# Performance work log

Hardware: AMD Instinct MI355X
Metric: run time of the kernel (lower is better)

The kernel has to match this reference:

```python
import jax, jax.numpy as jnp
import numpy as np

WS = 15
PAD = WS // 2
BN_EPS = 1e-5


def _unfold2d(a, ws):
    # a: (b, t, c, H, W) already padded -> (b, t, c, h, w, ws, ws), stride-1 windows
    h = a.shape[3] - ws + 1
    w = a.shape[4] - ws + 1
    ih = (jnp.arange(h)[:, None] + jnp.arange(ws)[None, :])  # (h, ws)
    iw = (jnp.arange(w)[:, None] + jnp.arange(ws)[None, :])  # (w, ws)
    return a[:, :, :, ih[:, None, :, None], iw[None, :, None, :]]


def setup_inputs() -> dict:
    key = jax.random.key(0)
    ks = jax.random.split(key, 11)
    b, t_mem, c, h, w = 2, 2, 256, 32, 32
    s = 0.05
    return {
        "x": jax.random.normal(ks[0], (b, c, h, w), jnp.float32),
        "mem": jax.random.normal(ks[1], (b, t_mem, c, h, w), jnp.float32),
        "w_qk": jax.random.normal(ks[2], (c // 8, c), jnp.float32) * s,
        "w_qv": jax.random.normal(ks[3], (c // 2, c), jnp.float32) * s,
        "w_mk": jax.random.normal(ks[4], (c // 8, c), jnp.float32) * s,
        "w_mv": jax.random.normal(ks[5], (c // 2, c), jnp.float32) * s,
        "w_smooth": jax.random.normal(ks[6], (c, c), jnp.float32) * s,
        "bn_gamma": jax.random.uniform(ks[7], (c,), jnp.float32, 0.5, 1.5),
        "bn_beta": jax.random.normal(ks[8], (c,), jnp.float32) * 0.1,
        "bn_mean": jnp.zeros((c,), jnp.float32),
        "bn_var": jnp.ones((c,), jnp.float32),
    }


def reference(x, mem, w_qk, w_qv, w_mk, w_mv, w_smooth, bn_gamma, bn_beta, bn_mean, bn_var):
    # mem <- cat([x, mem]) along time: (b, t, c, h, w)
    mem = jnp.concatenate([x[:, None], mem], axis=1)
    b, t, c, h, w = mem.shape

    # 1x1 convs == per-pixel matmuls
    query_k = jnp.einsum('bchw,oc->bohw', x, w_qk)          # (b, c/8, h, w)
    query_v = jnp.einsum('bchw,oc->bohw', x, w_qv)          # (b, c/2, h, w); Dropout2d(p=0) is identity
    mem_k = jnp.einsum('btchw,oc->btohw', mem, w_mk)        # (b, t, c/8, h, w)
    mem_v = jnp.einsum('btchw,oc->btohw', mem, w_mv)        # (b, t, c/2, h, w)

    pad = [(0, 0), (0, 0), (0, 0), (PAD, PAD), (PAD, PAD)]
    unf_k = _unfold2d(jnp.pad(mem_k, pad), WS)              # (b, t, c/8, h, w, ws, ws)
    unf_v = _unfold2d(jnp.pad(mem_v, pad), WS)              # (b, t, c/2, h, w, ws, ws)

    attn = jnp.einsum('bchw,btchwxy->bhwtxy', query_k, unf_k)
    attn = attn.reshape(b, h, w, t * WS * WS)
    # NOTE: faithful to original: softmax over dim=2 (the spatial w axis), not over keys
    attn = jax.nn.softmax(attn, axis=2)

    unf_v = jnp.transpose(unf_v, (0, 2, 3, 4, 1, 5, 6)).reshape(b, c // 2, h, w, t * WS * WS)
    mem_out = jnp.einsum('bhwk,bchwk->bchw', attn, unf_v)   # (b, c/2, h, w)

    feat = jnp.concatenate([query_v, mem_out], axis=1)      # (b, c, h, w)
    y = jnp.einsum('bchw,oc->bohw', feat, w_smooth)
    # BatchNorm2d in eval mode (running stats) + ReLU
    inv = bn_gamma / jnp.sqrt(bn_var + BN_EPS)
    y = y * inv[None, :, None, None] + (bn_beta - bn_mean * inv)[None, :, None, None]
    return jax.nn.relu(y)
```

## Files before the change

kernel.cpp:

```cpp
#include <hip/hip_runtime.h>
#include <math.h>

#define HWSZ 1024
#define HH 32
#define WW 32
#define C 256
#define CK 32
#define CV 128
#define T 3
#define WSZ 15
#define PADSZ 7
#define PADDED 46
#define PP (PADDED*PADDED)
#define KK (T*WSZ*WSZ)
#define B 2
#define NOUT 160
#define KC 32
#define PIXT 32
#define NPART 15

static const size_t OFF_QK   = 0;
static const size_t OFF_QV   = 65536;
static const size_t OFF_MK   = 327680;
static const size_t OFF_MV   = 733952;
static const size_t OFF_PART = 2359040;

__global__ __launch_bounds__(256) void k_proj(
    const float* __restrict__ x, const float* __restrict__ mem,
    const float* __restrict__ w_qk, const float* __restrict__ w_qv,
    const float* __restrict__ w_mk, const float* __restrict__ w_mv,
    float* __restrict__ ws)
{
    __shared__ float inT[KC][PIXT];
    __shared__ float wT[NOUT][KC + 1];

    int jb   = blockIdx.x >> 5;
    int rowt = blockIdx.x & 31;
    int tid  = threadIdx.x;
    int tx   = tid & 7;
    int ty   = tid >> 3;

    int b, t;
    const float *wk, *wv;
    bool isq;
    if (jb < 6) { b = jb / 3; t = jb % 3; wk = w_mk; wv = w_mv; isq = false; }
    else        { b = jb - 6; t = 0;      wk = w_qk; wv = w_qv; isq = true;  }

    const float* src = (t == 0)
        ? (x + ((size_t)b * C) * HWSZ)
        : (mem + ((size_t)(b * (T - 1) + (t - 1)) * C) * HWSZ);
    int hw0 = rowt * WW;

    float* mk = ws + OFF_MK;
    float* mv = ws + OFF_MV;
    size_t bt = (size_t)(b * T + t);

    if (!isq) {
        int yp = rowt + PADSZ;
        for (int f = tid; f < 448 + 1792; f += 256) {
            if (f < 448) {
                int c = f >> 4, sc = f & 15;
                if (sc < 14) {
                    int col = (sc < 7) ? sc : sc + 25;
                    mk[(bt * PP + yp * PADDED + col) * CK + c] = 0.f;
                }
            } else {
                int g = f - 448;
                int sc = g >> 7, c = g & 127;
                int col = (sc < 7) ? sc : sc + 25;
                mv[(bt * PP + yp * PADDED + col) * CV + c] = 0.f;
            }
        }
        if (rowt < 14) {
            int pr = (rowt < 7) ? rowt : rowt + 32;
            for (int f = tid; f < 1472 + 5888; f += 256) {
                if (f < 1472) {
                    int col = f >> 5, c = f & 31;
                    mk[(bt * PP + pr * PADDED + col) * CK + c] = 0.f;
                } else {
                    int g = f - 1472;
                    int col = g >> 7, c = g & 127;
                    mv[(bt * PP + pr * PADDED + col) * CV + c] = 0.f;
                }
            }
        }
    }

    float acc[5][4];
    #pragma unroll
    for (int j = 0; j < 5; j++)
        #pragma unroll
        for (int i = 0; i < 4; i++) acc[j][i] = 0.f;

    for (int c0 = 0; c0 < C; c0 += KC) {
        {
            int cc = tid >> 3;
            int p4 = (tid & 7) * 4;
            float4 v = *(const float4*)&src[(size_t)(c0 + cc) * HWSZ + hw0 + p4];
            inT[cc][p4 + 0] = v.x; inT[cc][p4 + 1] = v.y;
            inT[cc][p4 + 2] = v.z; inT[cc][p4 + 3] = v.w;
        }
        #pragma unroll
        for (int j = 0; j < 5; j++) {
            int f  = tid + j * 256;
            int o  = f >> 3;
            int c4 = (f & 7) * 4;
            const float* wr = (o < CK) ? (wk + (size_t)o * C) : (wv + (size_t)(o - CK) * C);
            float4 v = *(const float4*)&wr[c0 + c4];
            wT[o][c4 + 0] = v.x; wT[o][c4 + 1] = v.y;
            wT[o][c4 + 2] = v.z; wT[o][c4 + 3] = v.w;
        }
        __syncthreads();

        #pragma unroll 8
        for (int k = 0; k < KC; k++) {
            float4 iv = *(const float4*)&inT[k][tx * 4];
            #pragma unroll
            for (int j = 0; j < 5; j++) {
                float wv_ = wT[ty * 5 + j][k];
                acc[j][0] += wv_ * iv.x; acc[j][1] += wv_ * iv.y;
                acc[j][2] += wv_ * iv.z; acc[j][3] += wv_ * iv.w;
            }
        }
        __syncthreads();
    }

    int hq = rowt, yp = hq + PADSZ;
    #pragma unroll
    for (int j = 0; j < 5; j++) {
        int o = ty * 5 + j;
        #pragma unroll
        for (int i = 0; i < 4; i++) {
            int wq = tx * 4 + i;
            float v = acc[j][i];
            if (!isq) {
                int xp = wq + PADSZ;
                if (o < CK)
                    mk[(bt * PP + yp * PADDED + xp) * CK + o] = v;
                else
                    mv[(bt * PP + yp * PADDED + xp) * CV + (o - CK)] = v;
            } else {
                int hw = hq * WW + wq;
                if (o < CK) ws[OFF_QK + ((size_t)b * HWSZ + hw) * CK + o] = v;
                else        ws[OFF_QV + ((size_t)(b * CV + (o - CK))) * HWSZ + hw] = v;
            }
        }
    }
}

__global__ __launch_bounds__(256, 4) void k_attn_av(
    const float* __restrict__ qk, const float* __restrict__ mk,
    const float* __restrict__ mv, float* __restrict__ part)
{
    __shared__ float al[2][WSZ][WW];

    int blk = blockIdx.x;
    int xcd = blk & 7;
    int loc = blk >> 3;
    int xg  = loc % 5;
    int t   = (loc % 15) / 5;
    int bh  = xcd * 8 + loc / 15;
    int b   = bh >> 5, hq = bh & 31;
    int tid = threadIdx.x;

    const float* mkb = mk + (size_t)(b * T + t) * PP * CK;
    const float* mvb = mv + (size_t)(b * T + t) * PP * CV;

    int w  = tid & 31;
    int ty = tid >> 5;

    float4 q[8];
    {
        const float* qrow = qk + ((size_t)(b * HWSZ + hq * WW + w)) * CK;
        #pragma unroll
        for (int i = 0; i < 8; i++) q[i] = *(const float4*)&qrow[i * 4];
    }

    int cq = tid & 31;
    int wg = tid >> 5;
    int c0 = cq * 4;
    int w0 = wg * 4;

    float acc[4][4];
    #pragma unroll
    for (int ci = 0; ci < 4; ci++)
        #pragma unroll
        for (int wi = 0; wi < 4; wi++) acc[ci][wi] = 0.f;

    int yy0 = ty, yy1r = (ty + 8 < WSZ) ? ty + 8 : WSZ - 1;
    bool has1 = (ty + 8 < WSZ);

    #pragma unroll 1
    for (int xi = 0; xi < 3; xi++) {
        int xx = xg * 3 + xi;
        int buf = xi & 1;
        const float* mkrow = mkb + (size_t)(hq + xx) * PADDED * CK;
        const float* vrow  = mvb + (size_t)(hq + xx) * PADDED * CV + c0;

        float s0 = 0.f, s1 = 0.f;
        {
            const float* k0 = mkrow + (size_t)(w + yy0) * CK;
            const float* k1 = mkrow + (size_t)(w + yy1r) * CK;
            #pragma unroll
            for (int cc = 0; cc < 8; cc++) {
                float4 m0 = *(const float4*)&k0[cc * 4];
                float4 m1 = *(const float4*)&k1[cc * 4];
                s0 += q[cc].x * m0.x + q[cc].y * m0.y + q[cc].z * m0.z + q[cc].w * m0.w;
                s1 += q[cc].x * m1.x + q[cc].y * m1.y + q[cc].z * m1.z + q[cc].w * m1.w;
            }
        }

        float4 vw[18];
        #pragma unroll
        for (int i = 0; i < 18; i++)
            vw[i] = *(const float4*)&vrow[(size_t)(w0 + i) * CV];

        {
            float m0 = s0, m1 = s1;
            #pragma unroll
            for (int d = 1; d < 32; d <<= 1) {
                m0 = fmaxf(m0, __shfl_xor(m0, d, 32));
                m1 = fmaxf(m1, __shfl_xor(m1, d, 32));
            }
            float e0 = __expf(s0 - m0), e1 = __expf(s1 - m1);
            float t0 = e0, t1 = e1;
            #pragma unroll
            for (int d = 1; d < 32; d <<= 1) {
                t0 += __shfl_xor(t0, d, 32);
                t1 += __shfl_xor(t1, d, 32);
            }
            al[buf][yy0][w] = e0 / t0;
            if (has1) al[buf][yy1r][w] = e1 / t1;
        }
        __syncthreads();

        #pragma unroll
        for (int yy = 0; yy < WSZ; yy++) {
            float4 a4 = *(const float4*)&al[buf][yy][w0];
            #pragma unroll
            for (int wi = 0; wi < 4; wi++) {
                float av = (wi == 0) ? a4.x : (wi == 1) ? a4.y : (wi == 2) ? a4.z : a4.w;
                float4 vv = vw[yy + wi];
                acc[0][wi] += av * vv.x;
                acc[1][wi] += av * vv.y;
                acc[2][wi] += av * vv.z;
                acc[3][wi] += av * vv.w;
            }
        }
    }

    float* pbase = part + ((size_t)(bh * NPART + (t * 5 + xg)) * CV) * WW;
    #pragma unroll
    for (int ci = 0; ci < 4; ci++) {
        float4 r; r.x = acc[ci][0]; r.y = acc[ci][1]; r.z = acc[ci][2]; r.w = acc[ci][3];
        *(float4*)&pbase[(c0 + ci) * WW + w0] = r;
    }
}

__global__ __launch_bounds__(256) void k_out(
    const float* __restrict__ qv, const float* __restrict__ part,
    const float* __restrict__ wsm,
    const float* __restrict__ g, const float* __restrict__ bta,
    const float* __restrict__ mean, const float* __restrict__ var,
    float* __restrict__ out)
{
    __shared__ float inT[KC][PIXT];
    __shared__ float wTt[KC][132];

    int blk  = blockIdx.x;
    int oh   = blk & 1;
    int rowt = (blk >> 1) & 31;
    int b    = blk >> 6;
    int tid  = threadIdx.x;
    int tx   = tid & 7;
    int ty   = tid >> 3;
    int hw0  = rowt * WW;
    int obase = oh * 128;
    int bh   = b * HH + rowt;

    float acc[4][4];
    #pragma unroll
    for (int j = 0; j < 4; j++)
        #pragma unroll
        for (int i = 0; i < 4; i++) acc[j][i] = 0.f;

    for (int c0 = 0; c0 < C; c0 += KC) {
        {
            int cc = tid >> 3;
            int p4 = (tid & 7) * 4;
            float4 v;
            if (c0 < CV) {
                v = *(const float4*)&qv[((size_t)(b * CV + c0 + cc)) * HWSZ + hw0 + p4];
            } else {
                int cloc = (c0 - CV) + cc;
                const float* pb = part + ((size_t)bh * NPART) * CV * WW + cloc * WW + p4;
                float4 s = *(const float4*)pb;
                #pragma unroll
                for (int tg = 1; tg < NPART; tg++) {
                    float4 a = *(const float4*)&pb[(size_t)tg * CV * WW];
                    s.x += a.x; s.y += a.y; s.z += a.z; s.w += a.w;
                }
                v = s;
            }
            inT[cc][p4 + 0] = v.x; inT[cc][p4 + 1] = v.y;
            inT[cc][p4 + 2] = v.z; inT[cc][p4 + 3] = v.w;
        }
        #pragma unroll
        for (int j = 0; j < 4; j++) {
            int f  = tid + j * 256;
            int o  = f >> 3;
            int c4 = (f & 7) * 4;
            float4 v = *(const float4*)&wsm[(size_t)(obase + o) * C + c0 + c4];
            wTt[c4 + 0][o] = v.x; wTt[c4 + 1][o] = v.y;
            wTt[c4 + 2][o] = v.z; wTt[c4 + 3][o] = v.w;
        }
        __syncthreads();

        #pragma unroll 8
        for (int k = 0; k < KC; k++) {
            float4 iv  = *(const float4*)&inT[k][tx * 4];
            float4 wv4 = *(const float4*)&wTt[k][ty * 4];
            acc[0][0] += wv4.x * iv.x; acc[0][1] += wv4.x * iv.y;
            acc[0][2] += wv4.x * iv.z; acc[0][3] += wv4.x * iv.w;
            acc[1][0] += wv4.y * iv.x; acc[1][1] += wv4.y * iv.y;
            acc[1][2] += wv4.y * iv.z; acc[1][3] += wv4.y * iv.w;
            acc[2][0] += wv4.z * iv.x; acc[2][1] += wv4.z * iv.y;
            acc[2][2] += wv4.z * iv.z; acc[2][3] += wv4.z * iv.w;
            acc[3][0] += wv4.w * iv.x; acc[3][1] += wv4.w * iv.y;
            acc[3][2] += wv4.w * iv.z; acc[3][3] += wv4.w * iv.w;
        }
        __syncthreads();
    }

    #pragma unroll
    for (int j = 0; j < 4; j++) {
        int o = obase + ty * 4 + j;
        float inv = g[o] * rsqrtf(var[o] + 1e-5f);
        float sh  = bta[o] - mean[o] * inv;
        float4 r;
        r.x = fmaxf(acc[j][0] * inv + sh, 0.f);
        r.y = fmaxf(acc[j][1] * inv + sh, 0.f);
        r.z = fmaxf(acc[j][2] * inv + sh, 0.f);
        r.w = fmaxf(acc[j][3] * inv + sh, 0.f);
        *(float4*)&out[((size_t)(b * C + o)) * HWSZ + hw0 + tx * 4] = r;
    }
}

extern "C" void kernel_launch(void* const* d_in, const int* in_sizes, int n_in,
                              void* d_out, int out_size, void* d_ws, size_t ws_size,
                              hipStream_t stream) {
    const float* x    = (const float*)d_in[0];
    const float* mem  = (const float*)d_in[1];
    const float* w_qk = (const float*)d_in[2];
    const float* w_qv = (const float*)d_in[3];
    const float* w_mk = (const float*)d_in[4];
    const float* w_mv = (const float*)d_in[5];
    const float* wsm  = (const float*)d_in[6];
    const float* g    = (const float*)d_in[7];
    const float* bta  = (const float*)d_in[8];
    const float* mean = (const float*)d_in[9];
    const float* var  = (const float*)d_in[10];
    float* out = (float*)d_out;
    float* ws  = (float*)d_ws;

    k_proj<<<8 * 32, 256, 0, stream>>>(x, mem, w_qk, w_qv, w_mk, w_mv, ws);
    k_attn_av<<<960, 256, 0, stream>>>(ws + OFF_QK, ws + OFF_MK,
                                       ws + OFF_MV, ws + OFF_PART);
    k_out<<<B * 32 * 2, 256, 0, stream>>>(ws + OFF_QV, ws + OFF_PART, wsm,
                                          g, bta, mean, var, out);
}
```

Before: 102.0 us.

## Coarsen attention partials to 9 per row and retile output GEMM by pixel quarters

The attention kernel now gives each block 5 window rows instead of 3, so there are 9 partial sums per output row instead of 15. That cuts the partial-sum writes and the reduction reads in the output kernel, at the cost of fewer blocks (576 instead of 960). The output kernel now splits work by 8-pixel column chunks instead of halves of the output channels. Each block covers all 256 output channels for 8 pixels, which doubles the block count to 256 but makes every block load the full weight tile.

```diff
diff --git a/kernel.cpp b/kernel.cpp
--- a/kernel.cpp
+++ b/kernel.cpp
@@ -17,7 +17,7 @@
 #define NOUT 160
 #define KC 32
 #define PIXT 32
-#define NPART 15
+#define NPART 9
 
 static const size_t OFF_QK   = 0;
 static const size_t OFF_QV   = 65536;
@@ -157,9 +157,9 @@
     int blk = blockIdx.x;
     int xcd = blk & 7;
     int loc = blk >> 3;
-    int xg  = loc % 5;
-    int t   = (loc % 15) / 5;
-    int bh  = xcd * 8 + loc / 15;
+    int xg  = loc % 3;
+    int t   = (loc / 3) % 3;
+    int bh  = xcd * 8 + loc / 9;
     int b   = bh >> 5, hq = bh & 31;
     int tid = threadIdx.x;
 
@@ -191,8 +191,8 @@
     bool has1 = (ty + 8 < WSZ);
 
     #pragma unroll 1
-    for (int xi = 0; xi < 3; xi++) {
-        int xx = xg * 3 + xi;
+    for (int xi = 0; xi < 5; xi++) {
+        int xx = xg * 5 + xi;
         int buf = xi & 1;
         const float* mkrow = mkb + (size_t)(hq + xx) * PADDED * CK;
         const float* vrow  = mvb + (size_t)(hq + xx) * PADDED * CV + c0;
@@ -249,7 +249,7 @@
         }
     }
 
-    float* pbase = part + ((size_t)(bh * NPART + (t * 5 + xg)) * CV) * WW;
+    float* pbase = part + ((size_t)(bh * NPART + (t * 3 + xg)) * CV) * WW;
     #pragma unroll
     for (int ci = 0; ci < 4; ci++) {
         float4 r; r.x = acc[ci][0]; r.y = acc[ci][1]; r.z = acc[ci][2]; r.w = acc[ci][3];
@@ -264,36 +264,34 @@
     const float* __restrict__ mean, const float* __restrict__ var,
     float* __restrict__ out)
 {
-    __shared__ float inT[KC][PIXT];
-    __shared__ float wTt[KC][132];
+    __shared__ float inT[KC][8];
+    __shared__ float wTt[KC][260];
 
     int blk  = blockIdx.x;
-    int oh   = blk & 1;
-    int rowt = (blk >> 1) & 31;
-    int b    = blk >> 6;
+    int ph   = blk & 3;
+    int rowt = (blk >> 2) & 31;
+    int b    = blk >> 7;
     int tid  = threadIdx.x;
-    int tx   = tid & 7;
-    int ty   = tid >> 3;
-    int hw0  = rowt * WW;
-    int obase = oh * 128;
+    int tx   = tid & 3;
+    int ty   = tid >> 2;
+    int w0   = ph * 8;
+    int hw0  = rowt * WW + w0;
     int bh   = b * HH + rowt;
 
-    float acc[4][4];
-    #pragma unroll
-    for (int j = 0; j < 4; j++)
-        #pragma unroll
-        for (int i = 0; i < 4; i++) acc[j][i] = 0.f;
+    float acc[4][2];
+    #pragma unroll
+    for (int j = 0; j < 4; j++) { acc[j][0] = 0.f; acc[j][1] = 0.f; }
 
     for (int c0 = 0; c0 < C; c0 += KC) {
-        {
-            int cc = tid >> 3;
-            int p4 = (tid & 7) * 4;
+        if (tid < 64) {
+            int cc = tid >> 1, p4 = (tid & 1) * 4;
             float4 v;
             if (c0 < CV) {
                 v = *(const float4*)&qv[((size_t)(b * CV + c0 + cc)) * HWSZ + hw0 + p4];
             } else {
                 int cloc = (c0 - CV) + cc;
-                const float* pb = part + ((size_t)bh * NPART) * CV * WW + cloc * WW + p4;
+                const float* pb = part + ((size_t)bh * NPART) * CV * WW
+                                       + (size_t)cloc * WW + w0 + p4;
                 float4 s = *(const float4*)pb;
                 #pragma unroll
                 for (int tg = 1; tg < NPART; tg++) {
@@ -306,11 +304,11 @@
             inT[cc][p4 + 2] = v.z; inT[cc][p4 + 3] = v.w;
         }
         #pragma unroll
-        for (int j = 0; j < 4; j++) {
+        for (int j = 0; j < 8; j++) {
             int f  = tid + j * 256;
             int o  = f >> 3;
             int c4 = (f & 7) * 4;
-            float4 v = *(const float4*)&wsm[(size_t)(obase + o) * C + c0 + c4];
+            float4 v = *(const float4*)&wsm[(size_t)o * C + c0 + c4];
             wTt[c4 + 0][o] = v.x; wTt[c4 + 1][o] = v.y;
             wTt[c4 + 2][o] = v.z; wTt[c4 + 3][o] = v.w;
         }
@@ -318,31 +316,25 @@
 
         #pragma unroll 8
         for (int k = 0; k < KC; k++) {
-            float4 iv  = *(const float4*)&inT[k][tx * 4];
+            float2 iv  = *(const float2*)&inT[k][tx * 2];
             float4 wv4 = *(const float4*)&wTt[k][ty * 4];
             acc[0][0] += wv4.x * iv.x; acc[0][1] += wv4.x * iv.y;
-            acc[0][2] += wv4.x * iv.z; acc[0][3] += wv4.x * iv.w;
             acc[1][0] += wv4.y * iv.x; acc[1][1] += wv4.y * iv.y;
-            acc[1][2] += wv4.y * iv.z; acc[1][3] += wv4.y * iv.w;
             acc[2][0] += wv4.z * iv.x; acc[2][1] += wv4.z * iv.y;
-            acc[2][2] += wv4.z * iv.z; acc[2][3] += wv4.z * iv.w;
             acc[3][0] += wv4.w * iv.x; acc[3][1] += wv4.w * iv.y;
-            acc[3][2] += wv4.w * iv.z; acc[3][3] += wv4.w * iv.w;
         }
         __syncthreads();
     }
 
     #pragma unroll
     for (int j = 0; j < 4; j++) {
-        int o = obase + ty * 4 + j;
+        int o = ty * 4 + j;
         float inv = g[o] * rsqrtf(var[o] + 1e-5f);
         float sh  = bta[o] - mean[o] * inv;
-        float4 r;
+        float2 r;
         r.x = fmaxf(acc[j][0] * inv + sh, 0.f);
         r.y = fmaxf(acc[j][1] * inv + sh, 0.f);
-        r.z = fmaxf(acc[j][2] * inv + sh, 0.f);
-        r.w = fmaxf(acc[j][3] * inv + sh, 0.f);
-        *(float4*)&out[((size_t)(b * C + o)) * HWSZ + hw0 + tx * 4] = r;
+        *(float2*)&out[((size_t)(b * C + o)) * HWSZ + hw0 + tx * 2] = r;
     }
 }
 
@@ -364,8 +356,8 @@
     float* ws  = (float*)d_ws;
 
     k_proj<<<8 * 32, 256, 0, stream>>>(x, mem, w_qk, w_qv, w_mk, w_mv, ws);
-    k_attn_av<<<960, 256, 0, stream>>>(ws + OFF_QK, ws + OFF_MK,
+    k_attn_av<<<576, 256, 0, stream>>>(ws + OFF_QK, ws + OFF_MK,
                                        ws + OFF_MV, ws + OFF_PART);
-    k_out<<<B * 32 * 2, 256, 0, stream>>>(ws + OFF_QV, ws + OFF_PART, wsm,
+    k_out<<<B * 32 * 4, 256, 0, stream>>>(ws + OFF_QV, ws + OFF_PART, wsm,
                                           g, bta, mean, var, out);
 }
```

Result: slower. 108.7 us (+6.6%).
